# Performance work log

Hardware: AMD Instinct MI355X
Metric: run time of the kernel (lower is better)

## Reference

```python
import jax, jax.numpy as jnp
import numpy as np


def _mlp(h, W_in, b_in, W_hid, b_hid, W_out, b_out):
    # 392 -> 1000 -> (1000)x4 -> 392, ReLU between linear layers (NICE shift net)
    h = jax.nn.relu(h @ W_in + b_in)
    for i in range(W_hid.shape[0]):  # fixed small layer count, not a data dim
        h = jax.nn.relu(h @ W_hid[i] + b_hid[i])
    return h @ W_out + b_out


def setup_inputs() -> dict:
    key = jax.random.key(0)
    ks = jax.random.split(key, 4)
    B, D, MID = 4096, 784, 1000
    half = D // 2
    return {
        "x": jax.random.normal(ks[0], (B, D), jnp.float32),
        "log_det_J": jnp.zeros((1,), jnp.float32),
        "W_in": jax.random.normal(ks[1], (half, MID), jnp.float32) * 0.05,
        "b_in": jnp.zeros((MID,), jnp.float32),
        "W_hid": jax.random.normal(ks[2], (4, MID, MID), jnp.float32) * 0.03,
        "b_hid": jnp.zeros((4, MID), jnp.float32),
        "W_out": jax.random.normal(ks[3], (MID, half), jnp.float32) * 0.03,
        "b_out": jnp.zeros((half,), jnp.float32),
    }


def reference(x, log_det_J, W_in, b_in, W_hid, b_hid, W_out, b_out):
    # mask_config = 0: first = even columns, second = odd columns
    first = x[:, 0::2]   # (B, D/2)
    second = x[:, 1::2]  # (B, D/2)
    shift = _mlp(first, W_in, b_in, W_hid, b_hid, W_out, b_out)
    y_second = second + shift  # coupling_law (reverse=False)
    # interleave: y[:, 0::2] = first, y[:, 1::2] = y_second, in one strided write
    y = jnp.stack([first, y_second], axis=2).reshape(x.shape)
    return (y, log_det_J)
```

## Files before the change

### kernel.cpp

```cpp
#include <hip/hip_runtime.h>

typedef __bf16 bf16;
typedef __bf16 bf16x8 __attribute__((ext_vector_type(8)));
typedef float f32x4 __attribute__((ext_vector_type(4)));

#define M_TOT 4096
#define D_IN  784
#define HALF  392
#define MID   1000
#define K0PAD 448
#define NPAD  1024

__device__ __forceinline__ void g2l16(const bf16* g, bf16* l) {
  __builtin_amdgcn_global_load_lds(
      (__attribute__((address_space(1))) void*)(g),
      (__attribute__((address_space(3))) void*)(l),
      16, 0, 0);
}

__global__ void prep_k(const float* __restrict__ x, const float* __restrict__ ldj,
                       const float* __restrict__ W_in, const float* __restrict__ W_hid,
                       const float* __restrict__ W_out,
                       bf16* __restrict__ A0, bf16* __restrict__ WT0,
                       bf16* __restrict__ WTh, bf16* __restrict__ WT5,
                       float* __restrict__ y) {
  int b = blockIdx.x;
  int tid = threadIdx.x;
  if (b == 0 && tid == 0) y[(size_t)M_TOT * D_IN] = ldj[0];

  if (b < 8192) {
    int m = b >> 1;
    int k = (b & 1) * 256 + tid;
    if (k < K0PAD)
      A0[(size_t)m * K0PAD + k] = (k < HALF) ? (bf16)x[(size_t)m * D_IN + 2 * k] : (bf16)0.f;
    return;
  }
  int t = b - 8192;
  const float* W; bf16* WT; int K, N, Kpad, tn, tk;
  if (t < 448) {
    W = W_in; WT = WT0; K = HALF; N = MID; Kpad = K0PAD;
    tn = t & 31; tk = t >> 5;
  } else if (t < 448 + 4096) {
    int u = t - 448; int i = u >> 10; u &= 1023;
    W = W_hid + (size_t)i * MID * MID; WT = WTh + (size_t)i * NPAD * NPAD;
    K = MID; N = MID; Kpad = NPAD;
    tn = u & 31; tk = u >> 5;
  } else {
    int u = t - 4544;
    W = W_out; WT = WT5; K = MID; N = HALF; Kpad = NPAD;
    tn = u & 15; tk = u >> 4;
  }
  __shared__ float tb[32][33];
  int n0 = tn * 32, k0 = tk * 32;
  int tx = tid & 31, ty = tid >> 5;
#pragma unroll
  for (int r = 0; r < 4; ++r) {
    int k = k0 + ty + 8 * r, n = n0 + tx;
    tb[ty + 8 * r][tx] = (k < K && n < N) ? W[(size_t)k * N + n] : 0.f;
  }
  __syncthreads();
#pragma unroll
  for (int r = 0; r < 4; ++r) {
    int n = n0 + ty + 8 * r, k = k0 + tx;
    WT[(size_t)n * Kpad + k] = (bf16)tb[tx][ty + 8 * r];
  }
}

template <int BM, int BN, int EPI, int K>
__global__ __launch_bounds__(256, 4)
void gemm_k(const bf16* __restrict__ A, const bf16* __restrict__ BT,
            const float* __restrict__ bias, int bias_n,
            bf16* __restrict__ C,
            const float* __restrict__ x, float* __restrict__ y) {
  constexpr int BK = 64;
  constexpr int MT = BM / 32, NT = BN / 32;
  constexpr int KT = K / BK;
  __shared__ bf16 ldsA[BM * BK];
  __shared__ bf16 ldsB[BN * BK];
  const int tid = threadIdx.x, wave = tid >> 6, lane = tid & 63;
  const int bm = blockIdx.x, bn = blockIdx.y;

  const int srow = lane >> 3;
  const int sq = (lane & 7) ^ srow;
  const bf16* gA = A + ((size_t)bm * BM + wave * (BM / 4) + srow) * K + sq * 8;
  const bf16* gB = BT + ((size_t)bn * BN + wave * (BN / 4) + srow) * K + sq * 8;
  bf16* lA = &ldsA[wave * (BM / 4) * BK];
  bf16* lB = &ldsB[wave * (BN / 4) * BK];

  const int mlane = lane & 15, quad = lane >> 4;
  const int wm = (wave & 1) * (BM / 2), wn = (wave >> 1) * (BN / 2);
  const int axor = mlane & 7;
  const bf16* raBase = &ldsA[(wm + mlane) * BK];
  const bf16* rbBase = &ldsB[(wn + mlane) * BK];

  f32x4 acc[MT][NT] = {};

#pragma unroll
  for (int i = 0; i < BM / 32; ++i) g2l16(gA + (size_t)(8 * i) * K, lA + (8 * i) * BK);
#pragma unroll
  for (int i = 0; i < BN / 32; ++i) g2l16(gB + (size_t)(8 * i) * K, lB + (8 * i) * BK);

  for (int kt = 0; kt < KT; ++kt) {
    __syncthreads();
    bf16x8 af[2][MT], bfr[2][NT];
#pragma unroll
    for (int s = 0; s < 2; ++s) {
      const int co = ((s * 4 + quad) ^ axor) * 8;
#pragma unroll
      for (int i = 0; i < MT; ++i) af[s][i] = *(const bf16x8*)(raBase + i * 16 * BK + co);
#pragma unroll
      for (int i = 0; i < NT; ++i) bfr[s][i] = *(const bf16x8*)(rbBase + i * 16 * BK + co);
    }
    __syncthreads();
    if (kt + 1 < KT) {
      const size_t off = (size_t)(kt + 1) * BK;
#pragma unroll
      for (int i = 0; i < BM / 32; ++i) g2l16(gA + off + (size_t)(8 * i) * K, lA + (8 * i) * BK);
#pragma unroll
      for (int i = 0; i < BN / 32; ++i) g2l16(gB + off + (size_t)(8 * i) * K, lB + (8 * i) * BK);
    }
#pragma unroll
    for (int s = 0; s < 2; ++s)
#pragma unroll
      for (int mt = 0; mt < MT; ++mt)
#pragma unroll
        for (int nt = 0; nt < NT; ++nt)
          acc[mt][nt] = __builtin_amdgcn_mfma_f32_16x16x32_bf16(
              af[s][mt], bfr[s][nt], acc[mt][nt], 0, 0, 0);
  }

  const int ng0 = bn * BN + wn + mlane;
  const int mg0 = bm * BM + wm + quad * 4;

  if (EPI == 0) {
    float bv[NT];
#pragma unroll
    for (int nt = 0; nt < NT; ++nt) {
      int n = ng0 + nt * 16;
      bv[nt] = (n < bias_n) ? bias[n] : 0.f;
    }
#pragma unroll
    for (int mt = 0; mt < MT; ++mt)
#pragma unroll
      for (int nt = 0; nt < NT; ++nt)
#pragma unroll
        for (int r = 0; r < 4; ++r) {
          int m = mg0 + mt * 16 + r;
          int n = ng0 + nt * 16;
          float v = fmaxf(acc[mt][nt][r] + bv[nt], 0.f);
          C[(size_t)m * NPAD + n] = (bf16)v;
        }
  } else {
    const float2* x2 = (const float2*)x;
    float2* y2 = (float2*)y;
#pragma unroll
    for (int nt = 0; nt < NT; ++nt) {
      int n = ng0 + nt * 16;
      if (n < HALF) {
        float bb = bias[n];
#pragma unroll
        for (int mt = 0; mt < MT; ++mt)
#pragma unroll
          for (int r = 0; r < 4; ++r) {
            int m = mg0 + mt * 16 + r;
            size_t off = (size_t)m * (D_IN / 2) + n;
            float2 v = x2[off];
            v.y += acc[mt][nt][r] + bb;
            y2[off] = v;
          }
      }
    }
  }
}

extern "C" void kernel_launch(void* const* d_in, const int* in_sizes, int n_in,
                              void* d_out, int out_size, void* d_ws, size_t ws_size,
                              hipStream_t stream) {
  const float* x     = (const float*)d_in[0];
  const float* ldj   = (const float*)d_in[1];
  const float* W_in  = (const float*)d_in[2];
  const float* b_in  = (const float*)d_in[3];
  const float* W_hid = (const float*)d_in[4];
  const float* b_hid = (const float*)d_in[5];
  const float* W_out = (const float*)d_in[6];
  const float* b_out = (const float*)d_in[7];
  float* y = (float*)d_out;

  char* p = (char*)d_ws;
  bf16* A0  = (bf16*)(p + 0);
  bf16* H0  = (bf16*)(p + 3670016);
  bf16* H1  = (bf16*)(p + 12058624);
  bf16* WT0 = (bf16*)(p + 20447232);
  bf16* WTh = (bf16*)(p + 21364736);
  bf16* WT5 = (bf16*)(p + 29753344);

  prep_k<<<dim3(8192 + 5056), 256, 0, stream>>>(x, ldj, W_in, W_hid, W_out,
                                                A0, WT0, WTh, WT5, y);

  gemm_k<64, 64, 0, K0PAD><<<dim3(64, 16), 256, 0, stream>>>(A0, WT0, b_in, MID, H0, nullptr, nullptr);
  gemm_k<64, 64, 0, NPAD><<<dim3(64, 16), 256, 0, stream>>>(H0, WTh + 0 * (size_t)NPAD * NPAD, b_hid + 0 * MID, MID, H1, nullptr, nullptr);
  gemm_k<64, 64, 0, NPAD><<<dim3(64, 16), 256, 0, stream>>>(H1, WTh + 1 * (size_t)NPAD * NPAD, b_hid + 1 * MID, MID, H0, nullptr, nullptr);
  gemm_k<64, 64, 0, NPAD><<<dim3(64, 16), 256, 0, stream>>>(H0, WTh + 2 * (size_t)NPAD * NPAD, b_hid + 2 * MID, MID, H1, nullptr, nullptr);
  gemm_k<64, 64, 0, NPAD><<<dim3(64, 16), 256, 0, stream>>>(H1, WTh + 3 * (size_t)NPAD * NPAD, b_hid + 3 * MID, MID, H0, nullptr, nullptr);
  gemm_k<64, 64, 1, NPAD><<<dim3(64, 8), 256, 0, stream>>>(H0, WT5, b_out, HALF, nullptr, x, y);
}
```

Measured before the change: 175.2 us.

## Spread weight transposes into preceding GEMM launches and enlarge hidden tiles

Each hidden-layer weight transpose now runs as extra blocks appended to the previous GEMM's grid, so it overlaps with that layer's compute instead of sitting in one large prep kernel. The prep kernel now only builds A0 (with vectorized float4 loads and bf16x8 stores) and transposes W_in. The hidden-layer GEMMs use 128x64 tiles with a 1D grid and launch bounds of 2. This risks load imbalance between GEMM and transpose blocks, and lower occupancy from the larger tiles.

```diff
diff --git a/kernel.cpp b/kernel.cpp
--- a/kernel.cpp
+++ b/kernel.cpp
@@ -18,39 +18,9 @@
       16, 0, 0);
 }
 
-__global__ void prep_k(const float* __restrict__ x, const float* __restrict__ ldj,
-                       const float* __restrict__ W_in, const float* __restrict__ W_hid,
-                       const float* __restrict__ W_out,
-                       bf16* __restrict__ A0, bf16* __restrict__ WT0,
-                       bf16* __restrict__ WTh, bf16* __restrict__ WT5,
-                       float* __restrict__ y) {
-  int b = blockIdx.x;
-  int tid = threadIdx.x;
-  if (b == 0 && tid == 0) y[(size_t)M_TOT * D_IN] = ldj[0];
-
-  if (b < 8192) {
-    int m = b >> 1;
-    int k = (b & 1) * 256 + tid;
-    if (k < K0PAD)
-      A0[(size_t)m * K0PAD + k] = (k < HALF) ? (bf16)x[(size_t)m * D_IN + 2 * k] : (bf16)0.f;
-    return;
-  }
-  int t = b - 8192;
-  const float* W; bf16* WT; int K, N, Kpad, tn, tk;
-  if (t < 448) {
-    W = W_in; WT = WT0; K = HALF; N = MID; Kpad = K0PAD;
-    tn = t & 31; tk = t >> 5;
-  } else if (t < 448 + 4096) {
-    int u = t - 448; int i = u >> 10; u &= 1023;
-    W = W_hid + (size_t)i * MID * MID; WT = WTh + (size_t)i * NPAD * NPAD;
-    K = MID; N = MID; Kpad = NPAD;
-    tn = u & 31; tk = u >> 5;
-  } else {
-    int u = t - 4544;
-    W = W_out; WT = WT5; K = MID; N = HALF; Kpad = NPAD;
-    tn = u & 15; tk = u >> 4;
-  }
-  __shared__ float tb[32][33];
+__device__ __forceinline__ void wtrans_tile(const float* __restrict__ W, bf16* __restrict__ WT,
+                                            int K, int N, int Kpad, int tn, int tk,
+                                            float (*tb)[33], int tid) {
   int n0 = tn * 32, k0 = tk * 32;
   int tx = tid & 31, ty = tid >> 5;
 #pragma unroll
@@ -66,19 +36,61 @@
   }
 }
 
+__global__ void prep_k(const float* __restrict__ x, const float* __restrict__ ldj,
+                       const float* __restrict__ W_in,
+                       bf16* __restrict__ A0, bf16* __restrict__ WT0,
+                       float* __restrict__ y) {
+  __shared__ float tb[32][33];
+  const int b = blockIdx.x, tid = threadIdx.x;
+  if (b < 896) {
+    int g = b * 256 + tid;
+    int m = g / 56;
+    int kq = g - m * 56, k0 = kq * 8;
+    bf16x8 v;
+    if (k0 < HALF) {
+      const float4* xr = (const float4*)(x + (size_t)m * D_IN + 2 * k0);
+      float4 a0 = xr[0], a1 = xr[1], a2 = xr[2], a3 = xr[3];
+      v[0] = (bf16)a0.x; v[1] = (bf16)a0.z;
+      v[2] = (bf16)a1.x; v[3] = (bf16)a1.z;
+      v[4] = (bf16)a2.x; v[5] = (bf16)a2.z;
+      v[6] = (bf16)a3.x; v[7] = (bf16)a3.z;
+    } else {
+#pragma unroll
+      for (int j = 0; j < 8; ++j) v[j] = (bf16)0.f;
+    }
+    *(bf16x8*)(A0 + (size_t)m * K0PAD + k0) = v;
+    if (b == 0 && tid == 0) y[(size_t)M_TOT * D_IN] = ldj[0];
+    return;
+  }
+  int u = b - 896;
+  wtrans_tile(W_in, WT0, HALF, MID, K0PAD, u & 31, u >> 5, tb, tid);
+}
+
 template <int BM, int BN, int EPI, int K>
-__global__ __launch_bounds__(256, 4)
+__global__ __launch_bounds__(256, (BM > 64 ? 2 : 4))
 void gemm_k(const bf16* __restrict__ A, const bf16* __restrict__ BT,
             const float* __restrict__ bias, int bias_n,
             bf16* __restrict__ C,
-            const float* __restrict__ x, float* __restrict__ y) {
+            const float* __restrict__ x, float* __restrict__ y, int nb,
+            const float* __restrict__ Wx, bf16* __restrict__ WTx,
+            int wK, int wN, int wKpad, int wTN) {
   constexpr int BK = 64;
   constexpr int MT = BM / 32, NT = BN / 32;
   constexpr int KT = K / BK;
-  __shared__ bf16 ldsA[BM * BK];
-  __shared__ bf16 ldsB[BN * BK];
-  const int tid = threadIdx.x, wave = tid >> 6, lane = tid & 63;
-  const int bm = blockIdx.x, bn = blockIdx.y;
+  constexpr int NBM = M_TOT / BM;
+  alignas(16) __shared__ bf16 ldsA[BM * BK];
+  alignas(16) __shared__ bf16 ldsB[BN * BK];
+  const int tid = threadIdx.x;
+  const int id = blockIdx.x;
+
+  if (id >= nb) {
+    int u = id - nb;
+    wtrans_tile(Wx, WTx, wK, wN, wKpad, u % wTN, u / wTN, (float(*)[33])ldsA, tid);
+    return;
+  }
+
+  const int wave = tid >> 6, lane = tid & 63;
+  const int bm = id % NBM, bn = id / NBM;
 
   const int srow = lane >> 3;
   const int sq = (lane & 7) ^ srow;
@@ -194,13 +206,27 @@
   bf16* WTh = (bf16*)(p + 21364736);
   bf16* WT5 = (bf16*)(p + 29753344);
 
-  prep_k<<<dim3(8192 + 5056), 256, 0, stream>>>(x, ldj, W_in, W_hid, W_out,
-                                                A0, WT0, WTh, WT5, y);
-
-  gemm_k<64, 64, 0, K0PAD><<<dim3(64, 16), 256, 0, stream>>>(A0, WT0, b_in, MID, H0, nullptr, nullptr);
-  gemm_k<64, 64, 0, NPAD><<<dim3(64, 16), 256, 0, stream>>>(H0, WTh + 0 * (size_t)NPAD * NPAD, b_hid + 0 * MID, MID, H1, nullptr, nullptr);
-  gemm_k<64, 64, 0, NPAD><<<dim3(64, 16), 256, 0, stream>>>(H1, WTh + 1 * (size_t)NPAD * NPAD, b_hid + 1 * MID, MID, H0, nullptr, nullptr);
-  gemm_k<64, 64, 0, NPAD><<<dim3(64, 16), 256, 0, stream>>>(H0, WTh + 2 * (size_t)NPAD * NPAD, b_hid + 2 * MID, MID, H1, nullptr, nullptr);
-  gemm_k<64, 64, 0, NPAD><<<dim3(64, 16), 256, 0, stream>>>(H1, WTh + 3 * (size_t)NPAD * NPAD, b_hid + 3 * MID, MID, H0, nullptr, nullptr);
-  gemm_k<64, 64, 1, NPAD><<<dim3(64, 8), 256, 0, stream>>>(H0, WT5, b_out, HALF, nullptr, x, y);
-}
+  const size_t WH = (size_t)NPAD * NPAD;
+  const size_t WS = (size_t)MID * MID;
+
+  prep_k<<<dim3(896 + 448), 256, 0, stream>>>(x, ldj, W_in, A0, WT0, y);
+
+  gemm_k<128, 64, 0, K0PAD><<<dim3(512 + 1024), 256, 0, stream>>>(
+      A0, WT0, b_in, MID, H0, nullptr, nullptr, 512,
+      W_hid + 0 * WS, WTh + 0 * WH, MID, MID, NPAD, 32);
+  gemm_k<128, 64, 0, NPAD><<<dim3(512 + 1024), 256, 0, stream>>>(
+      H0, WTh + 0 * WH, b_hid + 0 * MID, MID, H1, nullptr, nullptr, 512,
+      W_hid + 1 * WS, WTh + 1 * WH, MID, MID, NPAD, 32);
+  gemm_k<128, 64, 0, NPAD><<<dim3(512 + 1024), 256, 0, stream>>>(
+      H1, WTh + 1 * WH, b_hid + 1 * MID, MID, H0, nullptr, nullptr, 512,
+      W_hid + 2 * WS, WTh + 2 * WH, MID, MID, NPAD, 32);
+  gemm_k<128, 64, 0, NPAD><<<dim3(512 + 1024), 256, 0, stream>>>(
+      H0, WTh + 2 * WH, b_hid + 2 * MID, MID, H1, nullptr, nullptr, 512,
+      W_hid + 3 * WS, WTh + 3 * WH, MID, MID, NPAD, 32);
+  gemm_k<128, 64, 0, NPAD><<<dim3(512 + 512), 256, 0, stream>>>(
+      H1, WTh + 3 * WH, b_hid + 3 * MID, MID, H0, nullptr, nullptr, 512,
+      W_out, WT5, MID, HALF, NPAD, 16);
+  gemm_k<64, 64, 1, NPAD><<<dim3(512), 256, 0, stream>>>(
+      H0, WT5, b_out, HALF, nullptr, x, y, 512,
+      nullptr, nullptr, 0, 0, 0, 1);
+}
```

Measured after the change: 173.4 us. About the same (-1.0%).

## Fuse six MLP GEMM launches into one persistent kernel with grid barriers

Applied to the files above, without the earlier changes.

Replaces the six separate GEMM launches with a single persistent kernel of 256 blocks that computes each layer with 128x128 tiles and synchronizes between layers through atomic-counter grid barriers. The input gather in prep is vectorized to read float4 and write eight bf16 values per thread. This removes per-launch overhead and tail gaps between layers and raises reuse per tile. In exchange it relies on all 256 blocks being co-resident, drops occupancy, and spins in the barriers.

```diff
diff --git a/kernel.cpp b/kernel.cpp
--- a/kernel.cpp
+++ b/kernel.cpp
@@ -10,6 +10,15 @@
 #define MID   1000
 #define K0PAD 448
 #define NPAD  1024
+#define NBLK  256
+
+#define OFF_A0  0
+#define OFF_H0  3670016
+#define OFF_H1  12058624
+#define OFF_WT0 20447232
+#define OFF_WTH 21364736
+#define OFF_WT5 29753344
+#define OFF_CNT 30801920
 
 __device__ __forceinline__ void g2l16(const bf16* g, bf16* l) {
   __builtin_amdgcn_global_load_lds(
@@ -18,29 +27,61 @@
       16, 0, 0);
 }
 
+__device__ __forceinline__ void wtrans_tile(const float* __restrict__ W, bf16* __restrict__ WT,
+                                            int K, int N, int Kpad, int tn, int tk,
+                                            float (*tb)[33], int tid) {
+  int n0 = tn * 32, k0 = tk * 32;
+  int tx = tid & 31, ty = tid >> 5;
+#pragma unroll
+  for (int r = 0; r < 4; ++r) {
+    int k = k0 + ty + 8 * r, n = n0 + tx;
+    tb[ty + 8 * r][tx] = (k < K && n < N) ? W[(size_t)k * N + n] : 0.f;
+  }
+  __syncthreads();
+#pragma unroll
+  for (int r = 0; r < 4; ++r) {
+    int n = n0 + ty + 8 * r, k = k0 + tx;
+    WT[(size_t)n * Kpad + k] = (bf16)tb[tx][ty + 8 * r];
+  }
+}
+
 __global__ void prep_k(const float* __restrict__ x, const float* __restrict__ ldj,
                        const float* __restrict__ W_in, const float* __restrict__ W_hid,
                        const float* __restrict__ W_out,
                        bf16* __restrict__ A0, bf16* __restrict__ WT0,
                        bf16* __restrict__ WTh, bf16* __restrict__ WT5,
-                       float* __restrict__ y) {
-  int b = blockIdx.x;
-  int tid = threadIdx.x;
-  if (b == 0 && tid == 0) y[(size_t)M_TOT * D_IN] = ldj[0];
-
-  if (b < 8192) {
-    int m = b >> 1;
-    int k = (b & 1) * 256 + tid;
-    if (k < K0PAD)
-      A0[(size_t)m * K0PAD + k] = (k < HALF) ? (bf16)x[(size_t)m * D_IN + 2 * k] : (bf16)0.f;
+                       float* __restrict__ y, unsigned* __restrict__ cnt) {
+  __shared__ float tb[32][33];
+  const int b = blockIdx.x, tid = threadIdx.x;
+  if (b < 896) {
+    if (b == 0) {
+      if (tid == 0) y[(size_t)M_TOT * D_IN] = ldj[0];
+      if (tid < 8) cnt[tid] = 0u;
+    }
+    int g = b * 256 + tid;
+    int m = g / 56;
+    int kq = g - m * 56, k0 = kq * 8;
+    bf16x8 v;
+    if (k0 < HALF) {
+      const float4* xr = (const float4*)(x + (size_t)m * D_IN + 2 * k0);
+      float4 a0 = xr[0], a1 = xr[1], a2 = xr[2], a3 = xr[3];
+      v[0] = (bf16)a0.x; v[1] = (bf16)a0.z;
+      v[2] = (bf16)a1.x; v[3] = (bf16)a1.z;
+      v[4] = (bf16)a2.x; v[5] = (bf16)a2.z;
+      v[6] = (bf16)a3.x; v[7] = (bf16)a3.z;
+    } else {
+#pragma unroll
+      for (int j = 0; j < 8; ++j) v[j] = (bf16)0.f;
+    }
+    *(bf16x8*)(A0 + (size_t)m * K0PAD + k0) = v;
     return;
   }
-  int t = b - 8192;
+  int t = b - 896;
   const float* W; bf16* WT; int K, N, Kpad, tn, tk;
   if (t < 448) {
     W = W_in; WT = WT0; K = HALF; N = MID; Kpad = K0PAD;
     tn = t & 31; tk = t >> 5;
-  } else if (t < 448 + 4096) {
+  } else if (t < 4544) {
     int u = t - 448; int i = u >> 10; u &= 1023;
     W = W_hid + (size_t)i * MID * MID; WT = WTh + (size_t)i * NPAD * NPAD;
     K = MID; N = MID; Kpad = NPAD;
@@ -50,40 +91,43 @@
     W = W_out; WT = WT5; K = MID; N = HALF; Kpad = NPAD;
     tn = u & 15; tk = u >> 4;
   }
-  __shared__ float tb[32][33];
-  int n0 = tn * 32, k0 = tk * 32;
-  int tx = tid & 31, ty = tid >> 5;
-#pragma unroll
-  for (int r = 0; r < 4; ++r) {
-    int k = k0 + ty + 8 * r, n = n0 + tx;
-    tb[ty + 8 * r][tx] = (k < K && n < N) ? W[(size_t)k * N + n] : 0.f;
-  }
+  wtrans_tile(W, WT, K, N, Kpad, tn, tk, tb, tid);
+}
+
+__device__ __forceinline__ void gbar(unsigned* c) {
   __syncthreads();
-#pragma unroll
-  for (int r = 0; r < 4; ++r) {
-    int n = n0 + ty + 8 * r, k = k0 + tx;
-    WT[(size_t)n * Kpad + k] = (bf16)tb[tx][ty + 8 * r];
-  }
+  if (threadIdx.x == 0) {
+    __threadfence();
+    __hip_atomic_fetch_add(c, 1u, __ATOMIC_RELEASE, __HIP_MEMORY_SCOPE_AGENT);
+    unsigned v = 0u; int it = 0;
+    do {
+      v = __hip_atomic_load(c, __ATOMIC_ACQUIRE, __HIP_MEMORY_SCOPE_AGENT);
+      if (++it > (1 << 22)) break;
+      __builtin_amdgcn_s_sleep(8);
+    } while (v < (unsigned)NBLK);
+    __threadfence();
+  }
+  __syncthreads();
 }
 
 template <int BM, int BN, int EPI, int K>
-__global__ __launch_bounds__(256, 4)
-void gemm_k(const bf16* __restrict__ A, const bf16* __restrict__ BT,
-            const float* __restrict__ bias, int bias_n,
-            bf16* __restrict__ C,
-            const float* __restrict__ x, float* __restrict__ y) {
+__device__ __forceinline__ void mlp_tile(
+    const bf16* __restrict__ A, const bf16* __restrict__ BT,
+    const float* __restrict__ bias, int bias_n, bf16* __restrict__ C,
+    const float* __restrict__ x, float* __restrict__ y,
+    bf16* ldsA, bf16* ldsB, int bm, int bn, int tid) {
   constexpr int BK = 64;
   constexpr int MT = BM / 32, NT = BN / 32;
   constexpr int KT = K / BK;
-  __shared__ bf16 ldsA[BM * BK];
-  __shared__ bf16 ldsB[BN * BK];
-  const int tid = threadIdx.x, wave = tid >> 6, lane = tid & 63;
-  const int bm = blockIdx.x, bn = blockIdx.y;
+  constexpr int AI = (BM / 4) / 8;
+  constexpr int BI = (BN / 4) / 8;
+  static_assert(K % BK == 0, "K % BK");
+  const int wave = tid >> 6, lane = tid & 63;
 
   const int srow = lane >> 3;
-  const int sq = (lane & 7) ^ srow;
-  const bf16* gA = A + ((size_t)bm * BM + wave * (BM / 4) + srow) * K + sq * 8;
-  const bf16* gB = BT + ((size_t)bn * BN + wave * (BN / 4) + srow) * K + sq * 8;
+  const int scol = lane & 7;
+  const bf16* gAb = A + ((size_t)bm * BM + wave * (BM / 4)) * K;
+  const bf16* gBb = BT + ((size_t)bn * BN + wave * (BN / 4)) * K;
   bf16* lA = &ldsA[wave * (BM / 4) * BK];
   bf16* lB = &ldsB[wave * (BN / 4) * BK];
 
@@ -95,10 +139,20 @@
 
   f32x4 acc[MT][NT] = {};
 
-#pragma unroll
-  for (int i = 0; i < BM / 32; ++i) g2l16(gA + (size_t)(8 * i) * K, lA + (8 * i) * BK);
-#pragma unroll
-  for (int i = 0; i < BN / 32; ++i) g2l16(gB + (size_t)(8 * i) * K, lB + (8 * i) * BK);
+  auto stage = [&](int koff) {
+#pragma unroll
+    for (int i = 0; i < AI; ++i) {
+      int r = i * 8 + srow;
+      g2l16(gAb + (size_t)r * K + koff + (scol ^ (r & 7)) * 8, lA + i * 8 * BK);
+    }
+#pragma unroll
+    for (int i = 0; i < BI; ++i) {
+      int r = i * 8 + srow;
+      g2l16(gBb + (size_t)r * K + koff + (scol ^ (r & 7)) * 8, lB + i * 8 * BK);
+    }
+  };
+
+  stage(0);
 
   for (int kt = 0; kt < KT; ++kt) {
     __syncthreads();
@@ -112,13 +166,7 @@
       for (int i = 0; i < NT; ++i) bfr[s][i] = *(const bf16x8*)(rbBase + i * 16 * BK + co);
     }
     __syncthreads();
-    if (kt + 1 < KT) {
-      const size_t off = (size_t)(kt + 1) * BK;
-#pragma unroll
-      for (int i = 0; i < BM / 32; ++i) g2l16(gA + off + (size_t)(8 * i) * K, lA + (8 * i) * BK);
-#pragma unroll
-      for (int i = 0; i < BN / 32; ++i) g2l16(gB + off + (size_t)(8 * i) * K, lB + (8 * i) * BK);
-    }
+    if (kt + 1 < KT) stage((kt + 1) * BK);
 #pragma unroll
     for (int s = 0; s < 2; ++s)
 #pragma unroll
@@ -171,6 +219,46 @@
       }
     }
   }
+}
+
+__global__ __launch_bounds__(256, 2)
+void mlp_k(const float* __restrict__ b_in, const float* __restrict__ b_hid,
+           const float* __restrict__ b_out,
+           const float* __restrict__ x, float* __restrict__ y,
+           char* __restrict__ ws) {
+  alignas(16) __shared__ bf16 ldsA[128 * 64];
+  alignas(16) __shared__ bf16 ldsB[128 * 64];
+
+  bf16* A0  = (bf16*)(ws + OFF_A0);
+  bf16* H0  = (bf16*)(ws + OFF_H0);
+  bf16* H1  = (bf16*)(ws + OFF_H1);
+  bf16* WT0 = (bf16*)(ws + OFF_WT0);
+  bf16* WTh = (bf16*)(ws + OFF_WTH);
+  bf16* WT5 = (bf16*)(ws + OFF_WT5);
+  unsigned* cnt = (unsigned*)(ws + OFF_CNT);
+  const size_t WH = (size_t)NPAD * NPAD;
+
+  const int tid = threadIdx.x;
+  const int lid = (blockIdx.x & 7) * 32 + (blockIdx.x >> 3);
+  const int bm = lid >> 3, bn = lid & 7;
+
+  mlp_tile<128, 128, 0, K0PAD>(A0, WT0, b_in, MID, H0, nullptr, nullptr,
+                               ldsA, ldsB, bm, bn, tid);
+  gbar(cnt + 0);
+  mlp_tile<128, 128, 0, NPAD>(H0, WTh + 0 * WH, b_hid + 0 * MID, MID, H1, nullptr, nullptr,
+                              ldsA, ldsB, bm, bn, tid);
+  gbar(cnt + 1);
+  mlp_tile<128, 128, 0, NPAD>(H1, WTh + 1 * WH, b_hid + 1 * MID, MID, H0, nullptr, nullptr,
+                              ldsA, ldsB, bm, bn, tid);
+  gbar(cnt + 2);
+  mlp_tile<128, 128, 0, NPAD>(H0, WTh + 2 * WH, b_hid + 2 * MID, MID, H1, nullptr, nullptr,
+                              ldsA, ldsB, bm, bn, tid);
+  gbar(cnt + 3);
+  mlp_tile<128, 128, 0, NPAD>(H1, WTh + 3 * WH, b_hid + 3 * MID, MID, H0, nullptr, nullptr,
+                              ldsA, ldsB, bm, bn, tid);
+  gbar(cnt + 4);
+  mlp_tile<128, 64, 1, NPAD>(H0, WT5, b_out, HALF, nullptr, x, y,
+                             ldsA, ldsB, bm, bn, tid);
 }
 
 extern "C" void kernel_launch(void* const* d_in, const int* in_sizes, int n_in,
@@ -185,22 +273,15 @@
   const float* W_out = (const float*)d_in[6];
   const float* b_out = (const float*)d_in[7];
   float* y = (float*)d_out;
-
   char* p = (char*)d_ws;
-  bf16* A0  = (bf16*)(p + 0);
-  bf16* H0  = (bf16*)(p + 3670016);
-  bf16* H1  = (bf16*)(p + 12058624);
-  bf16* WT0 = (bf16*)(p + 20447232);
-  bf16* WTh = (bf16*)(p + 21364736);
-  bf16* WT5 = (bf16*)(p + 29753344);
-
-  prep_k<<<dim3(8192 + 5056), 256, 0, stream>>>(x, ldj, W_in, W_hid, W_out,
-                                                A0, WT0, WTh, WT5, y);
-
-  gemm_k<64, 64, 0, K0PAD><<<dim3(64, 16), 256, 0, stream>>>(A0, WT0, b_in, MID, H0, nullptr, nullptr);
-  gemm_k<64, 64, 0, NPAD><<<dim3(64, 16), 256, 0, stream>>>(H0, WTh + 0 * (size_t)NPAD * NPAD, b_hid + 0 * MID, MID, H1, nullptr, nullptr);
-  gemm_k<64, 64, 0, NPAD><<<dim3(64, 16), 256, 0, stream>>>(H1, WTh + 1 * (size_t)NPAD * NPAD, b_hid + 1 * MID, MID, H0, nullptr, nullptr);
-  gemm_k<64, 64, 0, NPAD><<<dim3(64, 16), 256, 0, stream>>>(H0, WTh + 2 * (size_t)NPAD * NPAD, b_hid + 2 * MID, MID, H1, nullptr, nullptr);
-  gemm_k<64, 64, 0, NPAD><<<dim3(64, 16), 256, 0, stream>>>(H1, WTh + 3 * (size_t)NPAD * NPAD, b_hid + 3 * MID, MID, H0, nullptr, nullptr);
-  gemm_k<64, 64, 1, NPAD><<<dim3(64, 8), 256, 0, stream>>>(H0, WT5, b_out, HALF, nullptr, x, y);
-}
+
+  bf16* A0  = (bf16*)(p + OFF_A0);
+  bf16* WT0 = (bf16*)(p + OFF_WT0);
+  bf16* WTh = (bf16*)(p + OFF_WTH);
+  bf16* WT5 = (bf16*)(p + OFF_WT5);
+  unsigned* cnt = (unsigned*)(p + OFF_CNT);
+
+  prep_k<<<dim3(896 + 5056), 256, 0, stream>>>(x, ldj, W_in, W_hid, W_out,
+                                               A0, WT0, WTh, WT5, y, cnt);
+  mlp_k<<<dim3(NBLK), 256, 0, stream>>>(b_in, b_hid, b_out, x, y, p);
+}
```

Result: slower. 378.2 us (+115.9%).
